# Kernel tuning notes

Hardware: AMD Instinct MI355X
Metric: run time of the kernel (lower is better)

The kernel has to match this reference:

```python
import jax, jax.numpy as jnp
from jax import lax
import numpy as np

B, T, D_IN = 1024, 64, 1662
H1, H2, H3 = 64, 128, 64


def _lstm_layer(x, w_ih, w_hh, b_ih, b_hh):
    """PyTorch-convention single-layer LSTM. x: [B,T,D]; gate order i,f,g,o."""
    Bc = x.shape[0]
    H = w_hh.shape[1]
    # Precompute input contribution for all timesteps: [B,T,4H]
    xg = jnp.einsum('btd,gd->btg', x, w_ih) + b_ih + b_hh

    def step(carry, xt):
        h, c = carry
        gates = xt + h @ w_hh.T  # [B,4H]
        i, f, g, o = jnp.split(gates, 4, axis=-1)
        i = jax.nn.sigmoid(i)
        f = jax.nn.sigmoid(f)
        g = jnp.tanh(g)
        o = jax.nn.sigmoid(o)
        c = f * c + i * g
        h = o * jnp.tanh(c)
        return (h, c), h

    h0 = jnp.zeros((Bc, H), x.dtype)
    (_, _), hs = lax.scan(step, (h0, h0), jnp.swapaxes(xg, 0, 1))
    return jnp.swapaxes(hs, 0, 1)  # [B,T,H]


def setup_inputs() -> dict:
    key = jax.random.key(0)
    ks = jax.random.split(key, 20)

    def u(k, shape, fan):
        bound = 1.0 / np.sqrt(fan)
        return jax.random.uniform(k, shape, jnp.float32, -bound, bound)

    x = jax.random.normal(ks[0], (B, T, D_IN), jnp.float32)
    return {
        'x': x,
        'w_ih1': u(ks[1], (4 * H1, D_IN), H1), 'w_hh1': u(ks[2], (4 * H1, H1), H1),
        'b_ih1': u(ks[3], (4 * H1,), H1),      'b_hh1': u(ks[4], (4 * H1,), H1),
        'w_ih2': u(ks[5], (4 * H2, H1), H2),   'w_hh2': u(ks[6], (4 * H2, H2), H2),
        'b_ih2': u(ks[7], (4 * H2,), H2),      'b_hh2': u(ks[8], (4 * H2,), H2),
        'w_ih3': u(ks[9], (4 * H3, H2), H3),   'w_hh3': u(ks[10], (4 * H3, H3), H3),
        'b_ih3': u(ks[11], (4 * H3,), H3),     'b_hh3': u(ks[12], (4 * H3,), H3),
        'fc1_w': u(ks[13], (64, 64), 64),      'fc1_b': u(ks[14], (64,), 64),
        'fc2_w': u(ks[15], (32, 64), 64),      'fc2_b': u(ks[16], (32,), 64),
        'fc3_w': u(ks[17], (3, 32), 32),       'fc3_b': u(ks[18], (3,), 32),
    }


def reference(x, w_ih1, w_hh1, b_ih1, b_hh1,
              w_ih2, w_hh2, b_ih2, b_hh2,
              w_ih3, w_hh3, b_ih3, b_hh3,
              fc1_w, fc1_b, fc2_w, fc2_b, fc3_w, fc3_b):
    h = _lstm_layer(x, w_ih1, w_hh1, b_ih1, b_hh1)   # [B,T,64]
    h = _lstm_layer(h, w_ih2, w_hh2, b_ih2, b_hh2)   # [B,T,128]
    h = _lstm_layer(h, w_ih3, w_hh3, b_ih3, b_hh3)   # [B,T,64]
    h = h[:, -1, :]                                   # [B,64]
    h = jax.nn.relu(h @ fc1_w.T + fc1_b)
    h = jax.nn.relu(h @ fc2_w.T + fc2_b)
    return jax.nn.softmax(h @ fc3_w.T + fc3_b, axis=1)  # [B,3]
```

## Files before the change

kernel.cpp:

```cpp
#include <hip/hip_runtime.h>
#include <hip/hip_bf16.h>

#define B_SZ   1024
#define T_SZ   64
#define D_IN   1662
#define D_INP  1664
#define M_SZ   (B_SZ * T_SZ)

typedef __attribute__((ext_vector_type(8))) short short8;
typedef __attribute__((ext_vector_type(4))) float f32x4;
typedef unsigned short ushort_t;

__device__ __forceinline__ unsigned short f2bf(float f) {
    unsigned u = __builtin_bit_cast(unsigned, f);
    u += 0x7FFFu + ((u >> 16) & 1u);
    return (unsigned short)(u >> 16);
}
__device__ __forceinline__ float bf2f(ushort_t u) {
    return __builtin_bit_cast(float, (unsigned)u << 16);
}

#define GLD16(gp, lp) __builtin_amdgcn_global_load_lds(                        \
    (const __attribute__((address_space(1))) void*)(gp),                       \
    (__attribute__((address_space(3))) void*)(lp), 16, 0, 0)

__device__ __forceinline__ float sigmoid_f(float x) {
    return 1.0f / (1.0f + __expf(-x));
}
__device__ __forceinline__ float tanh_f(float x) {
    float a = fabsf(x);
    float e = __expf(2.0f * a);
    float r = 1.0f - 2.0f / (e + 1.0f);
    return copysignf(r, x);
}

__global__ __launch_bounds__(256) void convert_w1(
    const float* __restrict__ src, ushort_t* __restrict__ dst)
{
    constexpr int cpr = D_INP >> 3;
    const int total = 256 * cpr;
    const int stride = gridDim.x * blockDim.x;
    for (int idx = blockIdx.x * blockDim.x + threadIdx.x;
         idx < total; idx += stride) {
        const int row  = idx / cpr;
        const int base = (idx % cpr) << 3;
        const float* s = src + (size_t)row * D_IN;
        short8 o;
        #pragma unroll
        for (int j = 0; j < 4; ++j) {
            const int k = base + 2 * j;
            float2 v = make_float2(0.f, 0.f);
            if (k < D_IN) v = *(const float2*)(s + k);
            o[2 * j]     = (short)f2bf(v.x);
            o[2 * j + 1] = (short)f2bf(v.y);
        }
        *(short8*)(dst + (size_t)row * D_INP + base) = o;
    }
}

__global__ __launch_bounds__(256, 4) void gemm_l1(
    const float* __restrict__ A, const ushort_t* __restrict__ W,
    ushort_t* __restrict__ out)
{
    constexpr int K = D_IN, Kp = D_INP, G = 256;
    __shared__ __align__(16) ushort_t As[64 * 32];
    __shared__ __align__(16) ushort_t Ws[256 * 32];

    const int tid = threadIdx.x, lane = tid & 63, wid = tid >> 6;
    const int m0 = blockIdx.x * 64;

    const int arow  = tid >> 2;
    const int acolb = (tid & 3) * 8;
    const float* Abase = A + (size_t)(m0 + arow) * K + acolb;

    const size_t wlofs = (size_t)(lane >> 2) * Kp + (lane & 3) * 8;
    const ushort_t* Wg0 = W + (size_t)(wid * 64) * Kp + wlofs;
    const ushort_t* Wg1 = Wg0 + (size_t)16 * Kp;
    const ushort_t* Wg2 = Wg0 + (size_t)32 * Kp;
    const ushort_t* Wg3 = Wg0 + (size_t)48 * Kp;
    ushort_t* lw0 = &Ws[(wid * 64) * 32];
    ushort_t* lw1 = lw0 + 16 * 32;
    ushort_t* lw2 = lw0 + 32 * 32;
    ushort_t* lw3 = lw0 + 48 * 32;

    const int fr = lane & 15, kq = (lane >> 4) * 8;

    f32x4 acc[4][4] = {};
    const int nFull = K / 32;

    float2 av[4];
    #pragma unroll
    for (int j = 0; j < 4; ++j) av[j] = *(const float2*)(Abase + 2 * j);

    for (int it = 0; it <= nFull; ++it) {
        const int k0 = it * 32;
        __syncthreads();
        GLD16(Wg0 + k0, lw0); GLD16(Wg1 + k0, lw1);
        GLD16(Wg2 + k0, lw2); GLD16(Wg3 + k0, lw3);
        short8 pk;
        #pragma unroll
        for (int j = 0; j < 4; ++j) {
            pk[2 * j]     = (short)f2bf(av[j].x);
            pk[2 * j + 1] = (short)f2bf(av[j].y);
        }
        *(short8*)&As[arow * 32 + acolb] = pk;
        __syncthreads();

        if (it < nFull) {
            const int kn = (it + 1) * 32;
            if (it + 1 < nFull) {
                #pragma unroll
                for (int j = 0; j < 4; ++j)
                    av[j] = *(const float2*)(Abase + kn + 2 * j);
            } else {
                #pragma unroll
                for (int j = 0; j < 4; ++j) {
                    const int kk = kn + acolb + 2 * j;
                    av[j] = (kk < K) ? *(const float2*)(Abase + kn + 2 * j)
                                     : make_float2(0.f, 0.f);
                }
            }
        }

        short8 af[4], bfr[4];
        #pragma unroll
        for (int fm = 0; fm < 4; ++fm)
            af[fm] = *(const short8*)&As[(fm * 16 + fr) * 32 + kq];
        #pragma unroll
        for (int fn = 0; fn < 4; ++fn)
            bfr[fn] = *(const short8*)&Ws[(wid * 64 + fn * 16 + fr) * 32 + kq];
        #pragma unroll
        for (int fm = 0; fm < 4; ++fm)
            #pragma unroll
            for (int fn = 0; fn < 4; ++fn)
                acc[fm][fn] = __builtin_amdgcn_mfma_f32_16x16x32_bf16(
                    af[fm], bfr[fn], acc[fm][fn], 0, 0, 0);
    }

    const int rbase = (lane >> 4) * 4;
    #pragma unroll
    for (int fn = 0; fn < 4; ++fn) {
        const int g = wid * 64 + fn * 16 + fr;
        #pragma unroll
        for (int fm = 0; fm < 4; ++fm) {
            const int mbase = m0 + fm * 16 + rbase;
            #pragma unroll
            for (int j = 0; j < 4; ++j)
                out[(size_t)(mbase + j) * G + g] = f2bf(acc[fm][fn][j]);
        }
    }
}

__global__ __launch_bounds__(512, 2) void lstm3_gg(
    const ushort_t* __restrict__ xg1,
    const float* __restrict__ whh1,
    const float* __restrict__ bih1, const float* __restrict__ bhh1,
    const float* __restrict__ wih2, const float* __restrict__ whh2,
    const float* __restrict__ bih2, const float* __restrict__ bhh2,
    const float* __restrict__ wih3, const float* __restrict__ whh3,
    const float* __restrict__ bih3, const float* __restrict__ bhh3,
    float* __restrict__ hlast, int Tn)
{
    __shared__ ushort_t h1sh[2][16 * 64];
    __shared__ ushort_t h2sh[2][16 * 128];
    __shared__ ushort_t h3sh[2][16 * 64];
    __shared__ __align__(16) ushort_t xsh[2][1024];
    __shared__ __align__(16) float gsw[8][128 * 4];

    const int tid = threadIdx.x, lane = tid & 63, wid = tid >> 6;
    const int r0 = blockIdx.x * 4;
    const int fr = lane & 15, hi = lane >> 4, kq = hi * 8;

    int role, ubase, Hl;
    if (wid < 2)      { role = 1; ubase = wid * 32;       Hl = 64; }
    else if (wid < 6) { role = 2; ubase = (wid - 2) * 32; Hl = 128; }
    else              { role = 3; ubase = (wid - 6) * 32; Hl = 64; }

    short8 bregS[2][4][2];
    short8 bregL[2][4][4];
    #pragma unroll
    for (int ut = 0; ut < 2; ++ut)
        #pragma unroll
        for (int g = 0; g < 4; ++g) {
            const int uu = ubase + ut * 16 + fr;
            const float *pS, *pL = nullptr;
            if (role == 1)      { pS = whh1 + (size_t)(g * 64 + uu) * 64; }
            else if (role == 2) { pS = wih2 + (size_t)(g * 128 + uu) * 64;
                                  pL = whh2 + (size_t)(g * 128 + uu) * 128; }
            else                { pS = whh3 + (size_t)(g * 64 + uu) * 64;
                                  pL = wih3 + (size_t)(g * 64 + uu) * 128; }
            #pragma unroll
            for (int ks = 0; ks < 2; ++ks) {
                const float4 v0 = *(const float4*)(pS + ks * 32 + kq);
                const float4 v1 = *(const float4*)(pS + ks * 32 + kq + 4);
                short8 b;
                b[0] = (short)f2bf(v0.x); b[1] = (short)f2bf(v0.y);
                b[2] = (short)f2bf(v0.z); b[3] = (short)f2bf(v0.w);
                b[4] = (short)f2bf(v1.x); b[5] = (short)f2bf(v1.y);
                b[6] = (short)f2bf(v1.z); b[7] = (short)f2bf(v1.w);
                bregS[ut][g][ks] = b;
            }
            if (role >= 2) {
                #pragma unroll
                for (int ks = 0; ks < 4; ++ks) {
                    const float4 v0 = *(const float4*)(pL + ks * 32 + kq);
                    const float4 v1 = *(const float4*)(pL + ks * 32 + kq + 4);
                    short8 b;
                    b[0] = (short)f2bf(v0.x); b[1] = (short)f2bf(v0.y);
                    b[2] = (short)f2bf(v0.z); b[3] = (short)f2bf(v0.w);
                    b[4] = (short)f2bf(v1.x); b[5] = (short)f2bf(v1.y);
                    b[6] = (short)f2bf(v1.z); b[7] = (short)f2bf(v1.w);
                    bregL[ut][g][ks] = b;
                }
            }
        }

    float bias[2][4];
    {
        const float* bihp = (role == 1) ? bih1 : (role == 2) ? bih2 : bih3;
        const float* bhhp = (role == 1) ? bhh1 : (role == 2) ? bhh2 : bhh3;
        #pragma unroll
        for (int i = 0; i < 2; ++i) {
            const int unit = ubase + i * 16 + fr;
            #pragma unroll
            for (int g = 0; g < 4; ++g)
                bias[i][g] = bihp[g * Hl + unit] + bhhp[g * Hl + unit];
        }
    }

    for (int i = tid; i < 16 * 64; i += 512) {
        h1sh[0][i] = 0; h1sh[1][i] = 0;
        h3sh[0][i] = 0; h3sh[1][i] = 0;
    }
    for (int i = tid; i < 16 * 128; i += 512) { h2sh[0][i] = 0; h2sh[1][i] = 0; }

    if (tid < 128) {
        const int rw = tid >> 5, xc = (tid & 31) * 8;
        *(short8*)&xsh[0][rw * 256 + xc] =
            *(const short8*)(xg1 + ((size_t)(r0 + rw) * Tn) * 256 + xc);
    }

    float c[2] = {0.f, 0.f};
    __syncthreads();

    const int nSteps = Tn + 2;
    for (int s = 0; s < nSteps; ++s) {
        const int rb = s & 1, wb = rb ^ 1;

        if (wid < 2 && s + 1 < Tn) {
            const int rw = wid * 2 + (lane >> 5);
            const int xc = (lane & 31) * 8;
            GLD16(xg1 + ((size_t)(r0 + rw) * Tn + (s + 1)) * 256 + xc,
                  &xsh[wb][wid * 512]);
        }

        const bool act = (role == 1) ? (s < Tn)
                       : (role == 2) ? (s >= 1 && s <= Tn)
                                     : (s >= 2 && s <= Tn + 1);
        if (act) {
            short8 aS[2], aL[4];
            const ushort_t* srcS = (role == 3) ? h3sh[rb] : h1sh[rb];
            #pragma unroll
            for (int ks = 0; ks < 2; ++ks) {
                const int k0 = ks * 32 + kq;
                aS[ks] = *(const short8*)&srcS[fr * 64 + (k0 ^ ((fr & 7) << 3))];
            }
            if (role >= 2) {
                #pragma unroll
                for (int ks = 0; ks < 4; ++ks) {
                    const int k0 = ks * 32 + kq;
                    aL[ks] = *(const short8*)
                        &h2sh[rb][fr * 128 + (k0 ^ ((fr & 7) << 3))];
                }
            }

            #pragma unroll
            for (int ut = 0; ut < 2; ++ut)
                #pragma unroll
                for (int g = 0; g < 4; ++g) {
                    f32x4 acc = {};
                    #pragma unroll
                    for (int ks = 0; ks < 2; ++ks)
                        acc = __builtin_amdgcn_mfma_f32_16x16x32_bf16(
                            aS[ks], bregS[ut][g][ks], acc, 0, 0, 0);
                    if (role >= 2) {
                        #pragma unroll
                        for (int ks = 0; ks < 4; ++ks)
                            acc = __builtin_amdgcn_mfma_f32_16x16x32_bf16(
                                aL[ks], bregL[ut][g][ks], acc, 0, 0, 0);
                    }
                    if (hi == 0)
                        *(f32x4*)&gsw[wid][(g * 32 + ut * 16 + fr) * 4] = acc;
                }

            #pragma unroll
            for (int i = 0; i < 2; ++i) {
                const int uloc = i * 16 + fr;
                const int unit = ubase + uloc;
                float gi = gsw[wid][(0 * 32 + uloc) * 4 + hi] + bias[i][0];
                float gf = gsw[wid][(1 * 32 + uloc) * 4 + hi] + bias[i][1];
                float gg = gsw[wid][(2 * 32 + uloc) * 4 + hi] + bias[i][2];
                float go = gsw[wid][(3 * 32 + uloc) * 4 + hi] + bias[i][3];
                if (role == 1) {
                    const ushort_t* xb = &xsh[rb][hi * 256 + unit];
                    gi += bf2f(xb[0]);   gf += bf2f(xb[64]);
                    gg += bf2f(xb[128]); go += bf2f(xb[192]);
                }
                const float iv = sigmoid_f(gi);
                const float fv = sigmoid_f(gf);
                const float gv = tanh_f(gg);
                const float ov = sigmoid_f(go);
                c[i] = fmaf(fv, c[i], iv * gv);
                const float h = ov * tanh_f(c[i]);
                ushort_t* hdst = (role == 1) ? h1sh[wb]
                               : (role == 2) ? h2sh[wb] : h3sh[wb];
                hdst[hi * Hl + (unit ^ (hi << 3))] = f2bf(h);
                if (role == 3 && s == Tn + 1)
                    hlast[(size_t)(r0 + hi) * 64 + unit] = h;
            }
        }
        __syncthreads();
    }
}

__global__ __launch_bounds__(256) void head_kernel(
    const float* __restrict__ hlast,
    const float* __restrict__ w1, const float* __restrict__ b1,
    const float* __restrict__ w2, const float* __restrict__ b2,
    const float* __restrict__ w3, const float* __restrict__ b3,
    float* __restrict__ out)
{
    __shared__ float W1[64][64];
    __shared__ float W2[32][64];
    __shared__ float W3[3][32];
    __shared__ float hin[16][64];
    __shared__ float a1[16][64];
    __shared__ float a2[16][32];
    __shared__ float lg[16][3];

    const int tid = threadIdx.x;
    const int r0 = blockIdx.x * 16;

    for (int i = tid; i < 64 * 64; i += 256) W1[i >> 6][i & 63] = w1[i];
    for (int i = tid; i < 32 * 64; i += 256) W2[i >> 6][i & 63] = w2[i];
    for (int i = tid; i < 3 * 32; i += 256) W3[i >> 5][i & 31] = w3[i];
    for (int i = tid; i < 16 * 64; i += 256) {
        int r = i >> 6, u = i & 63;
        hin[r][u] = hlast[(size_t)(r0 + r) * 64 + u];
    }
    __syncthreads();

    for (int i = tid; i < 16 * 64; i += 256) {
        int r = i >> 6, j = i & 63;
        float s = b1[j];
        #pragma unroll
        for (int k = 0; k < 64; ++k) s = fmaf(hin[r][k], W1[j][k], s);
        a1[r][j] = fmaxf(s, 0.f);
    }
    __syncthreads();

    for (int i = tid; i < 16 * 32; i += 256) {
        int r = i >> 5, j = i & 31;
        float s = b2[j];
        #pragma unroll
        for (int k = 0; k < 64; ++k) s = fmaf(a1[r][k], W2[j][k], s);
        a2[r][j] = fmaxf(s, 0.f);
    }
    __syncthreads();

    for (int i = tid; i < 16 * 3; i += 256) {
        int r = i / 3, j = i % 3;
        float s = b3[j];
        #pragma unroll
        for (int k = 0; k < 32; ++k) s = fmaf(a2[r][k], W3[j][k], s);
        lg[r][j] = s;
    }
    __syncthreads();

    if (tid < 16) {
        float l0 = lg[tid][0], l1 = lg[tid][1], l2 = lg[tid][2];
        float m = fmaxf(l0, fmaxf(l1, l2));
        float e0 = __expf(l0 - m), e1 = __expf(l1 - m), e2 = __expf(l2 - m);
        float inv = 1.0f / (e0 + e1 + e2);
        out[(size_t)(r0 + tid) * 3 + 0] = e0 * inv;
        out[(size_t)(r0 + tid) * 3 + 1] = e1 * inv;
        out[(size_t)(r0 + tid) * 3 + 2] = e2 * inv;
    }
}

extern "C" void kernel_launch(void* const* d_in, const int* in_sizes, int n_in,
                              void* d_out, int out_size, void* d_ws, size_t ws_size,
                              hipStream_t stream)
{
    const float* x    = (const float*)d_in[0];
    const float* wih1 = (const float*)d_in[1];
    const float* whh1 = (const float*)d_in[2];
    const float* bih1 = (const float*)d_in[3];
    const float* bhh1 = (const float*)d_in[4];
    const float* wih2 = (const float*)d_in[5];
    const float* whh2 = (const float*)d_in[6];
    const float* bih2 = (const float*)d_in[7];
    const float* bhh2 = (const float*)d_in[8];
    const float* wih3 = (const float*)d_in[9];
    const float* whh3 = (const float*)d_in[10];
    const float* bih3 = (const float*)d_in[11];
    const float* bhh3 = (const float*)d_in[12];
    const float* f1w  = (const float*)d_in[13];
    const float* f1b  = (const float*)d_in[14];
    const float* f2w  = (const float*)d_in[15];
    const float* f2b  = (const float*)d_in[16];
    const float* f3w  = (const float*)d_in[17];
    const float* f3b  = (const float*)d_in[18];
    float* outp = (float*)d_out;

    char* wsb = (char*)d_ws;
    size_t off = 0;
    ushort_t* bufA  = (ushort_t*)(wsb + off); off += 33554432;
    float*    hlast = (float*)(wsb + off);    off += 262144;
    ushort_t* w1b   = (ushort_t*)(wsb + off);

    const int T = T_SZ;

    convert_w1<<<208, 256, 0, stream>>>(wih1, w1b);

    gemm_l1<<<M_SZ / 64, 256, 0, stream>>>(x, w1b, bufA);

    lstm3_gg<<<B_SZ / 4, 512, 0, stream>>>(
        bufA, whh1, bih1, bhh1,
        wih2, whh2, bih2, bhh2,
        wih3, whh3, bih3, bhh3,
        hlast, T);

    head_kernel<<<B_SZ / 16, 256, 0, stream>>>(
        hlast, f1w, f1b, f2w, f2b, f3w, f3b, outp);
}
```

Before: 356.3 us.

## Shrink layer-1 GEMM M-tile to 32 rows and swizzle LDS to avoid bank conflicts

The input-projection GEMM now computes 32 rows per block instead of 64, which doubles the grid and raises the occupancy target to 6 blocks per CU. The A tile in LDS is padded to a 40-element stride, and the W tile columns are XOR-swizzled so MFMA fragment reads avoid bank conflicts. Because the GEMM is memory-bound on the fp32 A stream, the aim is better latency hiding. The cost is that the bf16 weights are re-read from L2 twice as often.

```diff
diff --git a/kernel.cpp b/kernel.cpp
--- a/kernel.cpp
+++ b/kernel.cpp
@@ -8,6 +8,7 @@
 #define M_SZ   (B_SZ * T_SZ)
 
 typedef __attribute__((ext_vector_type(8))) short short8;
+typedef __attribute__((ext_vector_type(4))) short short4v;
 typedef __attribute__((ext_vector_type(4))) float f32x4;
 typedef unsigned short ushort_t;
 
@@ -58,79 +59,76 @@
     }
 }
 
-__global__ __launch_bounds__(256, 4) void gemm_l1(
+__global__ __launch_bounds__(256, 6) void gemm_l1(
     const float* __restrict__ A, const ushort_t* __restrict__ W,
     ushort_t* __restrict__ out)
 {
     constexpr int K = D_IN, Kp = D_INP, G = 256;
-    __shared__ __align__(16) ushort_t As[64 * 32];
+    constexpr int AS = 40;
+    __shared__ __align__(16) ushort_t As[32 * AS];
     __shared__ __align__(16) ushort_t Ws[256 * 32];
 
     const int tid = threadIdx.x, lane = tid & 63, wid = tid >> 6;
-    const int m0 = blockIdx.x * 64;
-
-    const int arow  = tid >> 2;
-    const int acolb = (tid & 3) * 8;
-    const float* Abase = A + (size_t)(m0 + arow) * K + acolb;
-
-    const size_t wlofs = (size_t)(lane >> 2) * Kp + (lane & 3) * 8;
-    const ushort_t* Wg0 = W + (size_t)(wid * 64) * Kp + wlofs;
-    const ushort_t* Wg1 = Wg0 + (size_t)16 * Kp;
-    const ushort_t* Wg2 = Wg0 + (size_t)32 * Kp;
-    const ushort_t* Wg3 = Wg0 + (size_t)48 * Kp;
-    ushort_t* lw0 = &Ws[(wid * 64) * 32];
-    ushort_t* lw1 = lw0 + 16 * 32;
-    ushort_t* lw2 = lw0 + 32 * 32;
-    ushort_t* lw3 = lw0 + 48 * 32;
+    const int m0 = blockIdx.x * 32;
+
+    const int arow = tid >> 3;
+    const int acol = (tid & 7) * 4;
+    const float* Abase = A + (size_t)(m0 + arow) * K + acol;
+
+    const int wr_loc = lane >> 2;
+    const int wq     = lane & 3;
+    const int wqx    = (wq ^ (wr_loc & 3)) * 8;
 
     const int fr = lane & 15, kq = (lane >> 4) * 8;
 
-    f32x4 acc[4][4] = {};
+    f32x4 acc[2][4] = {};
     const int nFull = K / 32;
 
-    float2 av[4];
-    #pragma unroll
-    for (int j = 0; j < 4; ++j) av[j] = *(const float2*)(Abase + 2 * j);
+    float4 av = *(const float4*)Abase;
 
     for (int it = 0; it <= nFull; ++it) {
         const int k0 = it * 32;
         __syncthreads();
-        GLD16(Wg0 + k0, lw0); GLD16(Wg1 + k0, lw1);
-        GLD16(Wg2 + k0, lw2); GLD16(Wg3 + k0, lw3);
-        short8 pk;
-        #pragma unroll
-        for (int j = 0; j < 4; ++j) {
-            pk[2 * j]     = (short)f2bf(av[j].x);
-            pk[2 * j + 1] = (short)f2bf(av[j].y);
-        }
-        *(short8*)&As[arow * 32 + acolb] = pk;
+        #pragma unroll
+        for (int c = 0; c < 4; ++c) {
+            const int row = wid * 64 + c * 16 + wr_loc;
+            GLD16(W + (size_t)row * Kp + k0 + wqx,
+                  &Ws[(wid * 64 + c * 16) * 32]);
+        }
+        {
+            short4v pk;
+            pk[0] = (short)f2bf(av.x); pk[1] = (short)f2bf(av.y);
+            pk[2] = (short)f2bf(av.z); pk[3] = (short)f2bf(av.w);
+            *(short4v*)&As[arow * AS + acol] = pk;
+        }
         __syncthreads();
 
         if (it < nFull) {
-            const int kn = (it + 1) * 32;
+            const int kn = k0 + 32;
             if (it + 1 < nFull) {
-                #pragma unroll
-                for (int j = 0; j < 4; ++j)
-                    av[j] = *(const float2*)(Abase + kn + 2 * j);
+                av = *(const float4*)(Abase + kn);
             } else {
+                float t[4];
                 #pragma unroll
                 for (int j = 0; j < 4; ++j) {
-                    const int kk = kn + acolb + 2 * j;
-                    av[j] = (kk < K) ? *(const float2*)(Abase + kn + 2 * j)
-                                     : make_float2(0.f, 0.f);
+                    const int kk = kn + acol + j;
+                    t[j] = (kk < K) ? Abase[kn + j] : 0.f;
                 }
-            }
-        }
-
-        short8 af[4], bfr[4];
-        #pragma unroll
-        for (int fm = 0; fm < 4; ++fm)
-            af[fm] = *(const short8*)&As[(fm * 16 + fr) * 32 + kq];
-        #pragma unroll
-        for (int fn = 0; fn < 4; ++fn)
-            bfr[fn] = *(const short8*)&Ws[(wid * 64 + fn * 16 + fr) * 32 + kq];
-        #pragma unroll
-        for (int fm = 0; fm < 4; ++fm)
+                av = make_float4(t[0], t[1], t[2], t[3]);
+            }
+        }
+
+        short8 af[2], bfr[4];
+        #pragma unroll
+        for (int fm = 0; fm < 2; ++fm)
+            af[fm] = *(const short8*)&As[(fm * 16 + fr) * AS + kq];
+        #pragma unroll
+        for (int fn = 0; fn < 4; ++fn) {
+            const int r = wid * 64 + fn * 16 + fr;
+            bfr[fn] = *(const short8*)&Ws[r * 32 + (kq ^ ((r & 3) * 8))];
+        }
+        #pragma unroll
+        for (int fm = 0; fm < 2; ++fm)
             #pragma unroll
             for (int fn = 0; fn < 4; ++fn)
                 acc[fm][fn] = __builtin_amdgcn_mfma_f32_16x16x32_bf16(
@@ -142,7 +140,7 @@
     for (int fn = 0; fn < 4; ++fn) {
         const int g = wid * 64 + fn * 16 + fr;
         #pragma unroll
-        for (int fm = 0; fm < 4; ++fm) {
+        for (int fm = 0; fm < 2; ++fm) {
             const int mbase = m0 + fm * 16 + rbase;
             #pragma unroll
             for (int j = 0; j < 4; ++j)
@@ -423,7 +421,7 @@
 
     convert_w1<<<208, 256, 0, stream>>>(wih1, w1b);
 
-    gemm_l1<<<M_SZ / 64, 256, 0, stream>>>(x, w1b, bufA);
+    gemm_l1<<<M_SZ / 32, 256, 0, stream>>>(x, w1b, bufA);
 
     lstm3_gg<<<B_SZ / 4, 512, 0, stream>>>(
         bufA, whh1, bih1, bhh1,
```

Result: slower. 440.9 us (+23.7%).

## Pad A tile, XOR-swizzle W tile in LDS, and double-buffer A prefetch

Applied to the files above, without the earlier changes.

Pads the A shared-memory tile row stride from 32 to 40 elements and applies an XOR swizzle to the weight tile's 16-byte slots, both to reduce LDS bank conflicts on fragment reads. The A global loads are now issued two iterations ahead through two register buffers, giving more latency hiding at the cost of extra registers. The K loop is unrolled by two with a fixed 52-iteration count.

```diff
diff --git a/kernel.cpp b/kernel.cpp
--- a/kernel.cpp
+++ b/kernel.cpp
@@ -63,7 +63,9 @@
     ushort_t* __restrict__ out)
 {
     constexpr int K = D_IN, Kp = D_INP, G = 256;
-    __shared__ __align__(16) ushort_t As[64 * 32];
+    constexpr int AS = 40;
+    constexpr int NIT = 52;
+    __shared__ __align__(16) ushort_t As[64 * AS];
     __shared__ __align__(16) ushort_t Ws[256 * 32];
 
     const int tid = threadIdx.x, lane = tid & 63, wid = tid >> 6;
@@ -73,8 +75,9 @@
     const int acolb = (tid & 3) * 8;
     const float* Abase = A + (size_t)(m0 + arow) * K + acolb;
 
-    const size_t wlofs = (size_t)(lane >> 2) * Kp + (lane & 3) * 8;
-    const ushort_t* Wg0 = W + (size_t)(wid * 64) * Kp + wlofs;
+    const int wr_loc = lane >> 2;
+    const int wslot  = ((lane & 3) ^ ((wr_loc >> 1) & 3)) * 8;
+    const ushort_t* Wg0 = W + (size_t)(wid * 64 + wr_loc) * Kp + wslot;
     const ushort_t* Wg1 = Wg0 + (size_t)16 * Kp;
     const ushort_t* Wg2 = Wg0 + (size_t)32 * Kp;
     const ushort_t* Wg3 = Wg0 + (size_t)48 * Kp;
@@ -86,56 +89,70 @@
     const int fr = lane & 15, kq = (lane >> 4) * 8;
 
     f32x4 acc[4][4] = {};
-    const int nFull = K / 32;
-
-    float2 av[4];
-    #pragma unroll
-    for (int j = 0; j < 4; ++j) av[j] = *(const float2*)(Abase + 2 * j);
-
-    for (int it = 0; it <= nFull; ++it) {
-        const int k0 = it * 32;
-        __syncthreads();
-        GLD16(Wg0 + k0, lw0); GLD16(Wg1 + k0, lw1);
-        GLD16(Wg2 + k0, lw2); GLD16(Wg3 + k0, lw3);
-        short8 pk;
-        #pragma unroll
-        for (int j = 0; j < 4; ++j) {
-            pk[2 * j]     = (short)f2bf(av[j].x);
-            pk[2 * j + 1] = (short)f2bf(av[j].y);
-        }
-        *(short8*)&As[arow * 32 + acolb] = pk;
-        __syncthreads();
-
-        if (it < nFull) {
-            const int kn = (it + 1) * 32;
-            if (it + 1 < nFull) {
-                #pragma unroll
-                for (int j = 0; j < 4; ++j)
-                    av[j] = *(const float2*)(Abase + kn + 2 * j);
-            } else {
-                #pragma unroll
-                for (int j = 0; j < 4; ++j) {
-                    const int kk = kn + acolb + 2 * j;
-                    av[j] = (kk < K) ? *(const float2*)(Abase + kn + 2 * j)
-                                     : make_float2(0.f, 0.f);
-                }
-            }
-        }
-
-        short8 af[4], bfr[4];
-        #pragma unroll
-        for (int fm = 0; fm < 4; ++fm)
-            af[fm] = *(const short8*)&As[(fm * 16 + fr) * 32 + kq];
-        #pragma unroll
-        for (int fn = 0; fn < 4; ++fn)
-            bfr[fn] = *(const short8*)&Ws[(wid * 64 + fn * 16 + fr) * 32 + kq];
-        #pragma unroll
-        for (int fm = 0; fm < 4; ++fm)
-            #pragma unroll
-            for (int fn = 0; fn < 4; ++fn)
-                acc[fm][fn] = __builtin_amdgcn_mfma_f32_16x16x32_bf16(
-                    af[fm], bfr[fn], acc[fm][fn], 0, 0, 0);
-    }
+
+    auto loadA = [&](int T, float2* av) {
+        if (T < NIT - 1) {
+            const int k = T * 32;
+            #pragma unroll
+            for (int j = 0; j < 4; ++j)
+                av[j] = *(const float2*)(Abase + k + 2 * j);
+        } else if (T == NIT - 1) {
+            const int k = T * 32;
+            #pragma unroll
+            for (int j = 0; j < 4; ++j) {
+                const int kk = k + acolb + 2 * j;
+                av[j] = (kk < K) ? *(const float2*)(Abase + k + 2 * j)
+                                 : make_float2(0.f, 0.f);
+            }
+        }
+    };
+
+    float2 av0[4], av1[4];
+    loadA(0, av0);
+    loadA(1, av1);
+
+#define G16_ITER(T, AV)                                                        \
+  do {                                                                         \
+    const int k0 = (T) * 32;                                                   \
+    __syncthreads();                             \
+    GLD16(Wg0 + k0, lw0); GLD16(Wg1 + k0, lw1);                                \
+    GLD16(Wg2 + k0, lw2); GLD16(Wg3 + k0, lw3);                                \
+    {                                                                          \
+        short8 pk;                                                             \
+        _Pragma("unroll")                                                      \
+        for (int j = 0; j < 4; ++j) {                                          \
+            pk[2 * j]     = (short)f2bf(AV[j].x);                              \
+            pk[2 * j + 1] = (short)f2bf(AV[j].y);                              \
+        }                                                                      \
+        *(short8*)&As[arow * AS + acolb] = pk;                                 \
+    }                                                                          \
+    __syncthreads();                            \
+    loadA((T) + 2, AV);                                   \
+    {                                                                          \
+        short8 af[4], bfr[4];                                                  \
+        _Pragma("unroll")                                                      \
+        for (int fm = 0; fm < 4; ++fm)                                         \
+            af[fm] = *(const short8*)&As[(fm * 16 + fr) * AS + kq];            \
+        _Pragma("unroll")                                                      \
+        for (int fn = 0; fn < 4; ++fn) {                                       \
+            const int r = wid * 64 + fn * 16 + fr;                             \
+            bfr[fn] = *(const short8*)                                         \
+                &Ws[r * 32 + (kq ^ (((r >> 1) & 3) * 8))];                     \
+        }                                                                      \
+        _Pragma("unroll")                                                      \
+        for (int fm = 0; fm < 4; ++fm)                                         \
+            _Pragma("unroll")                                                  \
+            for (int fn = 0; fn < 4; ++fn)                                     \
+                acc[fm][fn] = __builtin_amdgcn_mfma_f32_16x16x32_bf16(         \
+                    af[fm], bfr[fn], acc[fm][fn], 0, 0, 0);                    \
+    }                                                                          \
+  } while (0)
+
+    for (int tt = 0; tt < NIT / 2; ++tt) {
+        G16_ITER(2 * tt,     av0);
+        G16_ITER(2 * tt + 1, av1);
+    }
+#undef G16_ITER
 
     const int rbase = (lane >> 4) * 4;
     #pragma unroll
```

Result: slower. 366.8 us (+2.9%).

## Double-buffer LDS tiles in layer-1 GEMM and pad A tile rows

Applied to the files above, without the earlier changes.

Layer-1 input GEMM now keeps A and W tiles in two LDS buffers. The next tile's W global-to-LDS copy and A conversion are issued before the current tile's MFMAs, which cuts the two barriers per iteration to one. The A tile row stride is padded from 32 to 40 elements to reduce LDS bank conflicts. Doubled LDS use lowers the occupancy hint from 4 to 3 blocks per CU.

```diff
diff --git a/kernel.cpp b/kernel.cpp
--- a/kernel.cpp
+++ b/kernel.cpp
@@ -58,13 +58,15 @@
     }
 }
 
-__global__ __launch_bounds__(256, 4) void gemm_l1(
+__global__ __launch_bounds__(256, 3) void gemm_l1(
     const float* __restrict__ A, const ushort_t* __restrict__ W,
     ushort_t* __restrict__ out)
 {
     constexpr int K = D_IN, Kp = D_INP, G = 256;
-    __shared__ __align__(16) ushort_t As[64 * 32];
-    __shared__ __align__(16) ushort_t Ws[256 * 32];
+    constexpr int AS = 40;
+    constexpr int NIT = 52;
+    __shared__ __align__(16) ushort_t As[2][64 * AS];
+    __shared__ __align__(16) ushort_t Ws[2][256 * 32];
 
     const int tid = threadIdx.x, lane = tid & 63, wid = tid >> 6;
     const int m0 = blockIdx.x * 64;
@@ -78,63 +80,76 @@
     const ushort_t* Wg1 = Wg0 + (size_t)16 * Kp;
     const ushort_t* Wg2 = Wg0 + (size_t)32 * Kp;
     const ushort_t* Wg3 = Wg0 + (size_t)48 * Kp;
-    ushort_t* lw0 = &Ws[(wid * 64) * 32];
-    ushort_t* lw1 = lw0 + 16 * 32;
-    ushort_t* lw2 = lw0 + 32 * 32;
-    ushort_t* lw3 = lw0 + 48 * 32;
 
     const int fr = lane & 15, kq = (lane >> 4) * 8;
 
     f32x4 acc[4][4] = {};
-    const int nFull = K / 32;
 
     float2 av[4];
-    #pragma unroll
-    for (int j = 0; j < 4; ++j) av[j] = *(const float2*)(Abase + 2 * j);
-
-    for (int it = 0; it <= nFull; ++it) {
-        const int k0 = it * 32;
-        __syncthreads();
-        GLD16(Wg0 + k0, lw0); GLD16(Wg1 + k0, lw1);
-        GLD16(Wg2 + k0, lw2); GLD16(Wg3 + k0, lw3);
+    auto loadA = [&](int T) {
+        if (T < NIT - 1) {
+            const int k = T * 32;
+            #pragma unroll
+            for (int j = 0; j < 4; ++j)
+                av[j] = *(const float2*)(Abase + k + 2 * j);
+        } else if (T == NIT - 1) {
+            const int k = T * 32;
+            #pragma unroll
+            for (int j = 0; j < 4; ++j) {
+                const int kk = k + acolb + 2 * j;
+                av[j] = (kk < K) ? *(const float2*)(Abase + k + 2 * j)
+                                 : make_float2(0.f, 0.f);
+            }
+        }
+    };
+    auto writeAs = [&](int buf) {
         short8 pk;
         #pragma unroll
         for (int j = 0; j < 4; ++j) {
             pk[2 * j]     = (short)f2bf(av[j].x);
             pk[2 * j + 1] = (short)f2bf(av[j].y);
         }
-        *(short8*)&As[arow * 32 + acolb] = pk;
-        __syncthreads();
-
-        if (it < nFull) {
-            const int kn = (it + 1) * 32;
-            if (it + 1 < nFull) {
-                #pragma unroll
-                for (int j = 0; j < 4; ++j)
-                    av[j] = *(const float2*)(Abase + kn + 2 * j);
-            } else {
-                #pragma unroll
-                for (int j = 0; j < 4; ++j) {
-                    const int kk = kn + acolb + 2 * j;
-                    av[j] = (kk < K) ? *(const float2*)(Abase + kn + 2 * j)
-                                     : make_float2(0.f, 0.f);
-                }
-            }
+        *(short8*)&As[buf][arow * AS + acolb] = pk;
+    };
+    auto stageW = [&](int T, int buf) {
+        const int k0 = T * 32;
+        ushort_t* lw = &Ws[buf][(wid * 64) * 32];
+        GLD16(Wg0 + k0, lw);
+        GLD16(Wg1 + k0, lw + 16 * 32);
+        GLD16(Wg2 + k0, lw + 32 * 32);
+        GLD16(Wg3 + k0, lw + 48 * 32);
+    };
+
+    loadA(0);
+    stageW(0, 0);
+    writeAs(0);
+    loadA(1);
+    __syncthreads();
+
+    for (int t = 0; t < NIT; ++t) {
+        const int cb = t & 1, nb = cb ^ 1;
+
+        if (t + 1 < NIT) {
+            stageW(t + 1, nb);
+            writeAs(nb);
+            loadA(t + 2);
         }
 
         short8 af[4], bfr[4];
         #pragma unroll
         for (int fm = 0; fm < 4; ++fm)
-            af[fm] = *(const short8*)&As[(fm * 16 + fr) * 32 + kq];
+            af[fm] = *(const short8*)&As[cb][(fm * 16 + fr) * AS + kq];
         #pragma unroll
         for (int fn = 0; fn < 4; ++fn)
-            bfr[fn] = *(const short8*)&Ws[(wid * 64 + fn * 16 + fr) * 32 + kq];
+            bfr[fn] = *(const short8*)&Ws[cb][(wid * 64 + fn * 16 + fr) * 32 + kq];
         #pragma unroll
         for (int fm = 0; fm < 4; ++fm)
             #pragma unroll
             for (int fn = 0; fn < 4; ++fn)
                 acc[fm][fn] = __builtin_amdgcn_mfma_f32_16x16x32_bf16(
                     af[fm], bfr[fn], acc[fm][fn], 0, 0, 0);
+
+        __syncthreads();
     }
 
     const int rbase = (lane >> 4) * 4;
```

After: 392.7 us. 1.1x slower.
